# Kernel tuning notes

Hardware: AMD Instinct MI355X
Metric: run time of the kernel (lower is better)

The kernel has to match this reference:

```python
import jax, jax.numpy as jnp
import numpy as np

K_CODES, D_DIM = 512, 64


def setup_inputs() -> dict:
    key = jax.random.key(0)
    k1, k2 = jax.random.split(key)
    x = jax.random.normal(k1, (32, D_DIM, 64, 64), dtype=jnp.float32)  # NCHW
    weight = jax.random.uniform(k2, (K_CODES, D_DIM), minval=-1.0 / K_CODES,
                                maxval=1.0 / K_CODES, dtype=jnp.float32)
    return {"x": x, "weight": weight}


def reference(x, weight):
    K = weight.shape[0]
    xp = jnp.transpose(x, (0, 2, 3, 1))          # [B, H, W, D]
    flat = xp.reshape(-1, weight.shape[1])       # [N, D]
    dist = (jnp.sum(flat * flat, axis=1, keepdims=True)
            + jnp.sum(weight * weight, axis=1)
            - 2.0 * flat @ weight.T)
    idx = jnp.argmin(dist, axis=1)               # [N]
    enc = jax.nn.one_hot(idx, K, dtype=jnp.float32)   # [N, K] one-hot scatter
    quantized = (enc @ weight).reshape(xp.shape)      # matmul codebook lookup
    commit_loss = jnp.mean(jnp.square(jax.lax.stop_gradient(quantized) - xp))
    vq_loss = jnp.mean(jnp.square(quantized - jax.lax.stop_gradient(xp)))
    loss = vq_loss + 1.0 * commit_loss           # commitment_cost = 1.0
    quant_st = xp + jax.lax.stop_gradient(quantized - xp)  # straight-through
    return (loss, jnp.transpose(quant_st, (0, 3, 1, 2)), enc, idx)
```

## Files before the change

### kernel.cpp

```cpp
#include <hip/hip_runtime.h>
#include <cfloat>

#define KC 512
#define DD 64
#define HW 4096
#define NPIX 131072
#define QSIZE 8388608
#define PXB 128
#define NBLK (NPIX / PXB)
#define NTH 512
#define MARGIN 4.0e-3f

typedef short short8 __attribute__((ext_vector_type(8)));
typedef float f32x4 __attribute__((ext_vector_type(4)));
typedef float nfloat4 __attribute__((ext_vector_type(4)));
typedef unsigned long long u64;

__device__ __forceinline__ unsigned short bf16_rne(float f) {
    unsigned int u = __float_as_uint(f);
    u += 0x7FFFu + ((u >> 16) & 1u);
    return (unsigned short)(u >> 16);
}

__global__ __launch_bounds__(NTH, 2) void vq_fused(
    const float* __restrict__ x, const float* __restrict__ w,
    float* __restrict__ out_q, float* __restrict__ out_enc,
    float* __restrict__ out_idx, double* __restrict__ partial) {

  __shared__ uint4 wlds[4096];
  __shared__ float xlds[PXB * 65];
  __shared__ float w2s[KC];
  __shared__ u64 candm[PXB][8];
  __shared__ float Xs[PXB];
  __shared__ int sidx[PXB];
  __shared__ float sredf[8];

  const int tid = threadIdx.x;
  const int lane = tid & 63;
  const int wv = tid >> 6;
  const int bix = blockIdx.x;
  const int b = bix >> 5;
  const int p0 = (bix & 31) * PXB;
  const float* xg = x + (size_t)b * (DD * HW) + p0;

  for (int i = tid; i < PXB * DD; i += NTH) {
    int d = i >> 7, pp = i & 127;
    xlds[pp * 65 + d] = xg[(size_t)d * HW + pp];
  }

  {
    const int k = tid;
    const float* wk = w + k * DD;
    float r0 = __fmul_rn(wk[0], wk[0]), r1 = __fmul_rn(wk[1], wk[1]),
          r2 = __fmul_rn(wk[2], wk[2]), r3 = __fmul_rn(wk[3], wk[3]),
          r4 = __fmul_rn(wk[4], wk[4]), r5 = __fmul_rn(wk[5], wk[5]),
          r6 = __fmul_rn(wk[6], wk[6]), r7 = __fmul_rn(wk[7], wk[7]);
    #pragma unroll
    for (int i = 8; i < DD; i += 8) {
      r0 = __fadd_rn(r0, __fmul_rn(wk[i+0], wk[i+0]));
      r1 = __fadd_rn(r1, __fmul_rn(wk[i+1], wk[i+1]));
      r2 = __fadd_rn(r2, __fmul_rn(wk[i+2], wk[i+2]));
      r3 = __fadd_rn(r3, __fmul_rn(wk[i+3], wk[i+3]));
      r4 = __fadd_rn(r4, __fmul_rn(wk[i+4], wk[i+4]));
      r5 = __fadd_rn(r5, __fmul_rn(wk[i+5], wk[i+5]));
      r6 = __fadd_rn(r6, __fmul_rn(wk[i+6], wk[i+6]));
      r7 = __fadd_rn(r7, __fmul_rn(wk[i+7], wk[i+7]));
    }
    w2s[k] = __fadd_rn(__fadd_rn(__fadd_rn(r0, r1), __fadd_rn(r2, r3)),
                       __fadd_rn(__fadd_rn(r4, r5), __fadd_rn(r6, r7)));
  }

  for (int s = tid; s < 4096; s += NTH) {
    int ct = s >> 7, kc = (s >> 6) & 1, ln = s & 63;
    int n = ln & 15, q = ln >> 4;
    const float* wp = w + (ct * 16 + n) * DD + kc * 32 + q * 8;
    nfloat4 f0 = *(const nfloat4*)(wp);
    nfloat4 f1 = *(const nfloat4*)(wp + 4);
    uint4 u;
    u.x = (unsigned)bf16_rne(f0[0]) | ((unsigned)bf16_rne(f0[1]) << 16);
    u.y = (unsigned)bf16_rne(f0[2]) | ((unsigned)bf16_rne(f0[3]) << 16);
    u.z = (unsigned)bf16_rne(f1[0]) | ((unsigned)bf16_rne(f1[1]) << 16);
    u.w = (unsigned)bf16_rne(f1[2]) | ((unsigned)bf16_rne(f1[3]) << 16);
    wlds[s] = u;
  }
  for (int i = tid; i < PXB * 8; i += NTH) ((u64*)candm)[i] = 0;
  __syncthreads();

  if (tid < PXB) {
    const float* xr = &xlds[tid * 65];
    float r0 = __fmul_rn(xr[0], xr[0]), r1 = __fmul_rn(xr[1], xr[1]),
          r2 = __fmul_rn(xr[2], xr[2]), r3 = __fmul_rn(xr[3], xr[3]),
          r4 = __fmul_rn(xr[4], xr[4]), r5 = __fmul_rn(xr[5], xr[5]),
          r6 = __fmul_rn(xr[6], xr[6]), r7 = __fmul_rn(xr[7], xr[7]);
    #pragma unroll
    for (int i = 8; i < DD; i += 8) {
      r0 = __fadd_rn(r0, __fmul_rn(xr[i+0], xr[i+0]));
      r1 = __fadd_rn(r1, __fmul_rn(xr[i+1], xr[i+1]));
      r2 = __fadd_rn(r2, __fmul_rn(xr[i+2], xr[i+2]));
      r3 = __fadd_rn(r3, __fmul_rn(xr[i+3], xr[i+3]));
      r4 = __fadd_rn(r4, __fmul_rn(xr[i+4], xr[i+4]));
      r5 = __fadd_rn(r5, __fmul_rn(xr[i+5], xr[i+5]));
      r6 = __fadd_rn(r6, __fmul_rn(xr[i+6], xr[i+6]));
      r7 = __fadd_rn(r7, __fmul_rn(xr[i+7], xr[i+7]));
    }
    Xs[tid] = __fadd_rn(__fadd_rn(__fadd_rn(r0, r1), __fadd_rn(r2, r3)),
                        __fadd_rn(__fadd_rn(r4, r5), __fadd_rn(r6, r7)));
  }

  const int am = lane & 15, aq = lane >> 4;
  const float* arow = &xlds[(wv * 16 + am) * 65];
  short8 a0, a1;
  #pragma unroll
  for (int j = 0; j < 8; ++j) {
    a0[j] = (short)bf16_rne(-2.0f * arow[aq * 8 + j]);
    a1[j] = (short)bf16_rne(-2.0f * arow[32 + aq * 8 + j]);
  }

  const short8* wl8 = (const short8*)wlds;
  const int cn = lane & 15;

  float m0 = FLT_MAX, m1 = FLT_MAX, m2 = FLT_MAX, m3 = FLT_MAX;
  for (int ct = 0; ct < 32; ++ct) {
    float wk2 = w2s[ct * 16 + cn];
    f32x4 acc = {wk2, wk2, wk2, wk2};
    acc = __builtin_amdgcn_mfma_f32_16x16x32_bf16(a0, wl8[ct * 128 + lane], acc, 0, 0, 0);
    acc = __builtin_amdgcn_mfma_f32_16x16x32_bf16(a1, wl8[ct * 128 + 64 + lane], acc, 0, 0, 0);
    m0 = fminf(m0, acc[0]); m1 = fminf(m1, acc[1]);
    m2 = fminf(m2, acc[2]); m3 = fminf(m3, acc[3]);
  }
  #pragma unroll
  for (int s = 1; s < 16; s <<= 1) {
    m0 = fminf(m0, __shfl_xor(m0, s));
    m1 = fminf(m1, __shfl_xor(m1, s));
    m2 = fminf(m2, __shfl_xor(m2, s));
    m3 = fminf(m3, __shfl_xor(m3, s));
  }
  const float t0 = m0 + MARGIN, t1 = m1 + MARGIN,
              t2 = m2 + MARGIN, t3 = m3 + MARGIN;

  for (int ct = 0; ct < 32; ++ct) {
    float wk2 = w2s[ct * 16 + cn];
    f32x4 acc = {wk2, wk2, wk2, wk2};
    acc = __builtin_amdgcn_mfma_f32_16x16x32_bf16(a0, wl8[ct * 128 + lane], acc, 0, 0, 0);
    acc = __builtin_amdgcn_mfma_f32_16x16x32_bf16(a1, wl8[ct * 128 + 64 + lane], acc, 0, 0, 0);
    u64 bm0 = __ballot(acc[0] <= t0);
    u64 bm1 = __ballot(acc[1] <= t1);
    u64 bm2 = __ballot(acc[2] <= t2);
    u64 bm3 = __ballot(acc[3] <= t3);
    if (lane < 4) {
      u64 mk = (lane == 0) ? bm0 : (lane == 1) ? bm1 : (lane == 2) ? bm2 : bm3;
      int word = ct >> 2, sh = (ct & 3) * 16;
      #pragma unroll
      for (int q = 0; q < 4; ++q) {
        u64 bits = (mk >> (q * 16)) & 0xFFFFull;
        if (bits) candm[wv * 16 + q * 4 + lane][word] |= bits << sh;
      }
    }
  }
  __syncthreads();

  {
    const int px = tid >> 2, part = tid & 3;
    const float X = Xs[px];
    const float* xr = &xlds[px * 65];
    float bestd = FLT_MAX; int bk = 1 << 30;
    for (int wd = part * 2; wd < part * 2 + 2; ++wd) {
      u64 msk = candm[px][wd];
      while (msk) {
        int bit = __ffsll((unsigned long long)msk) - 1;
        msk &= msk - 1;
        int k = wd * 64 + bit;
        const float* wp = w + k * DD;
        float P = 0.f;
        #pragma unroll
        for (int dc = 0; dc < 16; ++dc) {
          nfloat4 w4 = *(const nfloat4*)(wp + dc * 4);
          P = __fmaf_rn(xr[dc * 4 + 0], w4[0], P);
          P = __fmaf_rn(xr[dc * 4 + 1], w4[1], P);
          P = __fmaf_rn(xr[dc * 4 + 2], w4[2], P);
          P = __fmaf_rn(xr[dc * 4 + 3], w4[3], P);
        }
        float dist = __fsub_rn(__fadd_rn(X, w2s[k]), __fadd_rn(P, P));
        if (dist < bestd || (dist == bestd && k < bk)) { bestd = dist; bk = k; }
      }
    }
    float od = __shfl_down(bestd, 1); int ok = __shfl_down(bk, 1);
    if ((lane & 3) < 3 && (od < bestd || (od == bestd && ok < bk))) { bestd = od; bk = ok; }
    od = __shfl_down(bestd, 2); ok = __shfl_down(bk, 2);
    if ((lane & 3) < 2 && (od < bestd || (od == bestd && ok < bk))) { bestd = od; bk = ok; }
    if (part == 0) { sidx[px] = bk; out_idx[bix * PXB + px] = (float)bk; }
  }
  __syncthreads();

  float lsum = 0.f;
  float* qb = out_q + (size_t)b * (DD * HW) + p0;
  for (int i = tid; i < PXB * DD; i += NTH) {
    int d = i >> 7, pp = i & 127;
    float qv = w[sidx[pp] * DD + d];
    float dv = qv - xlds[pp * 65 + d];
    lsum = __fmaf_rn(dv, dv, lsum);
    __builtin_nontemporal_store(qv, qb + (size_t)d * HW + pp);
  }
  #pragma unroll
  for (int off = 32; off > 0; off >>= 1) lsum += __shfl_down(lsum, off);
  if (lane == 0) sredf[wv] = lsum;
  __syncthreads();
  if (tid == 0) {
    double t = 0.0;
    #pragma unroll
    for (int i = 0; i < 8; ++i) t += (double)sredf[i];
    partial[bix] = t;
  }

  float* basep = out_enc + (size_t)bix * (PXB * KC);
  for (int t = tid; t < 16383; t += NTH) {
    int u = 3 + 4 * t;
    nfloat4 v;
    #pragma unroll
    for (int j = 0; j < 4; ++j) {
      int e = u + j;
      v[j] = (sidx[e >> 9] == (e & 511)) ? 1.0f : 0.0f;
    }
    __builtin_nontemporal_store(v, (nfloat4*)(basep + u));
  }
  if (tid < 3) basep[tid] = (sidx[0] == tid) ? 1.0f : 0.0f;
  else if (tid == 3) basep[PXB * KC - 1] = (sidx[127] == 511) ? 1.0f : 0.0f;
}

__global__ void finish_kernel(const double* __restrict__ partial,
                              float* __restrict__ out) {
  int t = threadIdx.x;
  double s = partial[t] + partial[t + 256] + partial[t + 512] + partial[t + 768];
  #pragma unroll
  for (int off = 32; off > 0; off >>= 1) s += __shfl_down(s, off);
  __shared__ double sr[4];
  if ((t & 63) == 0) sr[t >> 6] = s;
  __syncthreads();
  if (t == 0)
    out[0] = (float)(2.0 * (sr[0] + sr[1] + sr[2] + sr[3]) / (double)QSIZE);
}

extern "C" void kernel_launch(void* const* d_in, const int* in_sizes, int n_in,
                              void* d_out, int out_size, void* d_ws, size_t ws_size,
                              hipStream_t stream) {
  const float* x = (const float*)d_in[0];
  const float* w = (const float*)d_in[1];
  float* out = (float*)d_out;
  float* out_q = out + 1;
  float* out_enc = out_q + QSIZE;
  float* out_idx = out_enc + (size_t)NPIX * KC;

  double* partial = (double*)d_ws;

  vq_fused<<<NBLK, NTH, 0, stream>>>(x, w, out_q, out_enc, out_idx, partial);
  finish_kernel<<<1, 256, 0, stream>>>(partial, out);
}
```

Baseline: 440.9 us.

## Drop x LDS staging tile and read x directly from global to raise occupancy

Removes the 33KB shared-memory tile holding the block's pixel vectors and instead reads x directly from global memory (strided by HW) in the norm, A-fragment, rescoring and loss loops. Launch bounds go from 2 to 4 blocks per CU, so the lower LDS footprint can allow more resident blocks. One barrier is moved after the A-fragment loads. The trade-off is repeated global/L2 reads of x, some of them per-thread strided by HW, in place of cheap LDS accesses. There is also a risk of register spilling under the tighter launch bound.

```diff
diff --git a/kernel.cpp b/kernel.cpp
--- a/kernel.cpp
+++ b/kernel.cpp
@@ -22,13 +22,12 @@
     return (unsigned short)(u >> 16);
 }
 
-__global__ __launch_bounds__(NTH, 2) void vq_fused(
+__global__ __launch_bounds__(NTH, 4) void vq_fused(
     const float* __restrict__ x, const float* __restrict__ w,
     float* __restrict__ out_q, float* __restrict__ out_enc,
     float* __restrict__ out_idx, double* __restrict__ partial) {
 
   __shared__ uint4 wlds[4096];
-  __shared__ float xlds[PXB * 65];
   __shared__ float w2s[KC];
   __shared__ u64 candm[PXB][8];
   __shared__ float Xs[PXB];
@@ -41,12 +40,7 @@
   const int bix = blockIdx.x;
   const int b = bix >> 5;
   const int p0 = (bix & 31) * PXB;
-  const float* xg = x + (size_t)b * (DD * HW) + p0;
-
-  for (int i = tid; i < PXB * DD; i += NTH) {
-    int d = i >> 7, pp = i & 127;
-    xlds[pp * 65 + d] = xg[(size_t)d * HW + pp];
-  }
+  const float* xt = x + (size_t)b * (DD * HW) + p0;
 
   {
     const int k = tid;
@@ -84,37 +78,38 @@
     wlds[s] = u;
   }
   for (int i = tid; i < PXB * 8; i += NTH) ((u64*)candm)[i] = 0;
-  __syncthreads();
 
   if (tid < PXB) {
-    const float* xr = &xlds[tid * 65];
-    float r0 = __fmul_rn(xr[0], xr[0]), r1 = __fmul_rn(xr[1], xr[1]),
-          r2 = __fmul_rn(xr[2], xr[2]), r3 = __fmul_rn(xr[3], xr[3]),
-          r4 = __fmul_rn(xr[4], xr[4]), r5 = __fmul_rn(xr[5], xr[5]),
-          r6 = __fmul_rn(xr[6], xr[6]), r7 = __fmul_rn(xr[7], xr[7]);
+    const float* xp = xt + tid;
+    float r0 = __fmul_rn(xp[0*HW], xp[0*HW]), r1 = __fmul_rn(xp[1*HW], xp[1*HW]),
+          r2 = __fmul_rn(xp[2*HW], xp[2*HW]), r3 = __fmul_rn(xp[3*HW], xp[3*HW]),
+          r4 = __fmul_rn(xp[4*HW], xp[4*HW]), r5 = __fmul_rn(xp[5*HW], xp[5*HW]),
+          r6 = __fmul_rn(xp[6*HW], xp[6*HW]), r7 = __fmul_rn(xp[7*HW], xp[7*HW]);
     #pragma unroll
     for (int i = 8; i < DD; i += 8) {
-      r0 = __fadd_rn(r0, __fmul_rn(xr[i+0], xr[i+0]));
-      r1 = __fadd_rn(r1, __fmul_rn(xr[i+1], xr[i+1]));
-      r2 = __fadd_rn(r2, __fmul_rn(xr[i+2], xr[i+2]));
-      r3 = __fadd_rn(r3, __fmul_rn(xr[i+3], xr[i+3]));
-      r4 = __fadd_rn(r4, __fmul_rn(xr[i+4], xr[i+4]));
-      r5 = __fadd_rn(r5, __fmul_rn(xr[i+5], xr[i+5]));
-      r6 = __fadd_rn(r6, __fmul_rn(xr[i+6], xr[i+6]));
-      r7 = __fadd_rn(r7, __fmul_rn(xr[i+7], xr[i+7]));
+      r0 = __fadd_rn(r0, __fmul_rn(xp[(size_t)(i+0)*HW], xp[(size_t)(i+0)*HW]));
+      r1 = __fadd_rn(r1, __fmul_rn(xp[(size_t)(i+1)*HW], xp[(size_t)(i+1)*HW]));
+      r2 = __fadd_rn(r2, __fmul_rn(xp[(size_t)(i+2)*HW], xp[(size_t)(i+2)*HW]));
+      r3 = __fadd_rn(r3, __fmul_rn(xp[(size_t)(i+3)*HW], xp[(size_t)(i+3)*HW]));
+      r4 = __fadd_rn(r4, __fmul_rn(xp[(size_t)(i+4)*HW], xp[(size_t)(i+4)*HW]));
+      r5 = __fadd_rn(r5, __fmul_rn(xp[(size_t)(i+5)*HW], xp[(size_t)(i+5)*HW]));
+      r6 = __fadd_rn(r6, __fmul_rn(xp[(size_t)(i+6)*HW], xp[(size_t)(i+6)*HW]));
+      r7 = __fadd_rn(r7, __fmul_rn(xp[(size_t)(i+7)*HW], xp[(size_t)(i+7)*HW]));
     }
     Xs[tid] = __fadd_rn(__fadd_rn(__fadd_rn(r0, r1), __fadd_rn(r2, r3)),
                         __fadd_rn(__fadd_rn(r4, r5), __fadd_rn(r6, r7)));
   }
 
   const int am = lane & 15, aq = lane >> 4;
-  const float* arow = &xlds[(wv * 16 + am) * 65];
+  const float* xa = xt + wv * 16 + am;
   short8 a0, a1;
   #pragma unroll
   for (int j = 0; j < 8; ++j) {
-    a0[j] = (short)bf16_rne(-2.0f * arow[aq * 8 + j]);
-    a1[j] = (short)bf16_rne(-2.0f * arow[32 + aq * 8 + j]);
-  }
+    a0[j] = (short)bf16_rne(-2.0f * xa[(size_t)(aq * 8 + j) * HW]);
+    a1[j] = (short)bf16_rne(-2.0f * xa[(size_t)(32 + aq * 8 + j) * HW]);
+  }
+
+  __syncthreads();
 
   const short8* wl8 = (const short8*)wlds;
   const int cn = lane & 15;
@@ -162,7 +157,7 @@
   {
     const int px = tid >> 2, part = tid & 3;
     const float X = Xs[px];
-    const float* xr = &xlds[px * 65];
+    const float* xr = xt + px;
     float bestd = FLT_MAX; int bk = 1 << 30;
     for (int wd = part * 2; wd < part * 2 + 2; ++wd) {
       u64 msk = candm[px][wd];
@@ -175,10 +170,10 @@
         #pragma unroll
         for (int dc = 0; dc < 16; ++dc) {
           nfloat4 w4 = *(const nfloat4*)(wp + dc * 4);
-          P = __fmaf_rn(xr[dc * 4 + 0], w4[0], P);
-          P = __fmaf_rn(xr[dc * 4 + 1], w4[1], P);
-          P = __fmaf_rn(xr[dc * 4 + 2], w4[2], P);
-          P = __fmaf_rn(xr[dc * 4 + 3], w4[3], P);
+          P = __fmaf_rn(xr[(size_t)(dc * 4 + 0) * HW], w4[0], P);
+          P = __fmaf_rn(xr[(size_t)(dc * 4 + 1) * HW], w4[1], P);
+          P = __fmaf_rn(xr[(size_t)(dc * 4 + 2) * HW], w4[2], P);
+          P = __fmaf_rn(xr[(size_t)(dc * 4 + 3) * HW], w4[3], P);
         }
         float dist = __fsub_rn(__fadd_rn(X, w2s[k]), __fadd_rn(P, P));
         if (dist < bestd || (dist == bestd && k < bk)) { bestd = dist; bk = k; }
@@ -188,7 +183,10 @@
     if ((lane & 3) < 3 && (od < bestd || (od == bestd && ok < bk))) { bestd = od; bk = ok; }
     od = __shfl_down(bestd, 2); ok = __shfl_down(bk, 2);
     if ((lane & 3) < 2 && (od < bestd || (od == bestd && ok < bk))) { bestd = od; bk = ok; }
-    if (part == 0) { sidx[px] = bk; out_idx[bix * PXB + px] = (float)bk; }
+    if (part == 0) {
+      sidx[px] = bk;
+      out_idx[bix * PXB + px] = (float)bk;
+    }
   }
   __syncthreads();
 
@@ -197,7 +195,7 @@
   for (int i = tid; i < PXB * DD; i += NTH) {
     int d = i >> 7, pp = i & 127;
     float qv = w[sidx[pp] * DD + d];
-    float dv = qv - xlds[pp * 65 + d];
+    float dv = qv - xt[(size_t)d * HW + pp];
     lsum = __fmaf_rn(dv, dv, lsum);
     __builtin_nontemporal_store(qv, qb + (size_t)d * HW + pp);
   }
```

Result: faster. 391.3 us (-11.3%).
